# Performance work log

Measured on AMD Instinct MI355X. Metric: run time of the kernel, lower is better.

The kernel has to match this reference:

```python
import jax, jax.numpy as jnp
import numpy as np

B, Q, C, N, H, W = 2, 4096, 256, 6, 64, 96
HEADS, POINTS = 8, 4


def _grid_sample(img, grid):
    # img: [G, C, H, W]; grid: [G, P, 2] in [-1,1]
    # bilinear, align_corners=False, padding_mode='zeros' (matches F.grid_sample)
    G, Cc, Hh, Ww = img.shape
    gx = (grid[..., 0] + 1.0) * (Ww / 2.0) - 0.5
    gy = (grid[..., 1] + 1.0) * (Hh / 2.0) - 0.5
    x0f = jnp.floor(gx)
    y0f = jnp.floor(gy)
    wx = (gx - x0f)[:, None, :]
    wy = (gy - y0f)[:, None, :]
    x0 = x0f.astype(jnp.int32)
    y0 = y0f.astype(jnp.int32)
    flat = img.reshape(G, Cc, Hh * Ww)

    def gather(xi, yi):
        valid = ((xi >= 0) & (xi < Ww) & (yi >= 0) & (yi < Hh))
        idx = jnp.clip(yi, 0, Hh - 1) * Ww + jnp.clip(xi, 0, Ww - 1)
        v = jnp.take_along_axis(flat, idx[:, None, :], axis=2)  # [G,C,P]
        return v * valid[:, None, :].astype(img.dtype)

    v00 = gather(x0, y0)
    v01 = gather(x0 + 1, y0)
    v10 = gather(x0, y0 + 1)
    v11 = gather(x0 + 1, y0 + 1)
    return (v00 * (1 - wx) * (1 - wy) + v01 * wx * (1 - wy)
            + v10 * (1 - wx) * wy + v11 * wx * wy)


def setup_inputs() -> dict:
    key = jax.random.key(0)
    ks = jax.random.split(key, 12)
    query = jax.random.normal(ks[0], (B, Q, C), dtype=jnp.float32)
    query_coords = jax.random.uniform(ks[1], (B, Q, 3), dtype=jnp.float32)
    image_feats = jax.random.normal(ks[2], (B, N, C, H, W), dtype=jnp.float32)
    # realistic f-theta fisheye intrinsics for 1280x1080 images
    Kmat = np.array([[500.0, 0.0, 640.0], [0.0, 500.0, 540.0], [0.0, 0.0, 1.0]], dtype=np.float32)
    intrinsics = jnp.asarray(np.tile(Kmat, (B, N, 1, 1)))
    # inverse extrinsics: identity rotation, cameras 3m behind the voxel volume (cam_z > 0)
    E = np.tile(np.eye(4, dtype=np.float32), (B, N, 1, 1))
    for n in range(N):
        E[:, n, 0, 3] = 0.2 * n - 0.5
        E[:, n, 2, 3] = 3.0
    inv_extrinsics = jnp.asarray(E)
    s = 1.0 / np.sqrt(C)
    W_off = jax.random.normal(ks[3], (C, N * HEADS * POINTS * 2), dtype=jnp.float32) * 0.02
    b_off = jnp.zeros((N * HEADS * POINTS * 2,), dtype=jnp.float32)
    W_attn = jax.random.normal(ks[4], (C, N * HEADS * POINTS), dtype=jnp.float32) * s
    b_attn = jnp.zeros((N * HEADS * POINTS,), dtype=jnp.float32)
    W_val = jax.random.normal(ks[5], (C, C), dtype=jnp.float32) * s
    b_val = jax.random.normal(ks[6], (C,), dtype=jnp.float32) * 0.01
    W_out = jax.random.normal(ks[7], (C, C), dtype=jnp.float32) * s
    b_out = jax.random.normal(ks[8], (C,), dtype=jnp.float32) * 0.01
    return {"query": query, "query_coords": query_coords, "image_feats": image_feats,
            "intrinsics": intrinsics, "inv_extrinsics": inv_extrinsics,
            "W_off": W_off, "b_off": b_off, "W_attn": W_attn, "b_attn": b_attn,
            "W_val": W_val, "b_val": b_val, "W_out": W_out, "b_out": b_out}


def reference(query, query_coords, image_feats, intrinsics, inv_extrinsics,
              W_off, b_off, W_attn, b_attn, W_val, b_val, W_out, b_out):
    Bq, Qq, Cq = query.shape
    _, Nn, _, Hh, Ww = image_feats.shape
    hd = Cq // HEADS
    # ---- reference points: voxel coords -> world -> camera -> f-theta image ----
    xmin, ymin, zmin, xmax, ymax, zmax = -3.6, -3.0, -0.7, 3.6, 3.0, 2.5
    rx = query_coords[..., 0] * (xmax - xmin) + xmin
    ry = query_coords[..., 1] * (ymax - ymin) + ymin
    rz = query_coords[..., 2] * (zmax - zmin) + zmin
    world = jnp.stack([rx, ry, rz, jnp.ones_like(rx)], axis=-1)  # [B,Q,4]
    cam = jnp.einsum('bnij,bqj->bnqi', inv_extrinsics, world)    # [B,N,Q,4]
    cxp, cyp, czp = cam[..., 0], cam[..., 1], cam[..., 2]
    r3d = jnp.sqrt(cxp * cxp + cyp * cyp + 1e-8)
    theta = jnp.arctan2(r3d, czp)
    phi = jnp.arctan2(cyp, cxp)
    fx = intrinsics[:, :, 0, 0][..., None]
    cx0 = intrinsics[:, :, 0, 2][..., None]
    cy0 = intrinsics[:, :, 1, 2][..., None]
    r_img = fx * theta
    u = r_img * jnp.cos(phi) + cx0
    v = r_img * jnp.sin(phi) + cy0
    origH, origW = 1080, 1280
    ref = jnp.stack([2.0 * u / (origW - 1) - 1.0, 2.0 * v / (origH - 1) - 1.0], axis=-1)  # [B,N,Q,2]
    fov = ((czp > 0) & (theta < 1.372)).astype(query.dtype)      # [B,N,Q]
    # ---- offsets + attention weights ----
    offs = jnp.tanh((query @ W_off + b_off).reshape(Bq, Qq, Nn, HEADS, POINTS, 2)) * 0.5
    aw = (query @ W_attn + b_attn).reshape(Bq, Qq, Nn, HEADS, POINTS)
    aw = aw * jnp.transpose(fov, (0, 2, 1))[..., None, None]
    aw = jax.nn.softmax(aw, axis=-1)
    # ---- value projection ----
    val = jnp.einsum('bnchw,cd->bnhwd', image_feats, W_val) + b_val  # [B,N,H,W,C]
    val = val.reshape(Bq, Nn, Hh, Ww, HEADS, hd)
    # ---- sampling locations ----
    locs = ref[:, :, :, None, None, :] + jnp.transpose(offs, (0, 2, 1, 3, 4, 5))  # [B,N,Q,h,p,2]
    v_all = jnp.transpose(val, (0, 1, 4, 5, 2, 3)).reshape(Bq * Nn * HEADS, hd, Hh, Ww)
    locs_all = jnp.transpose(locs, (0, 1, 3, 2, 4, 5)).reshape(Bq * Nn * HEADS, Qq * POINTS, 2)
    sampled = _grid_sample(v_all, locs_all).reshape(Bq, Nn, HEADS, hd, Qq, POINTS)
    sampled = jnp.transpose(sampled, (0, 4, 1, 2, 5, 3))  # [B,Q,N,heads,points,hd]
    weighted = jnp.sum(sampled * aw[..., None], axis=4)   # [B,Q,N,heads,hd]
    out = weighted.sum(axis=2).reshape(Bq, Qq, Cq)
    return out @ W_out + b_out
```

## Files before the change

### kernel.cpp

```cpp
#include <hip/hip_runtime.h>
#include <math.h>

#define Bb 2
#define Qq 4096
#define Cc 256
#define Nn 6
#define Hh 64
#define Ww 96
#define HEADS 8
#define POINTS 4
#define HW (Hh*Ww)
#define BQ (Bb*Qq)

#define WS_VAL   0
#define WS_WTF   9437184
#define WS_WCHF  9469952
#define WS_WCLF  9543680
#define WS_WOTF  9617408
#define WS_LOCS  18874368
#define WS_AW    22020096
#define WS_REFF  23592960
#define WS_WSUM  23740416

typedef __attribute__((ext_vector_type(8))) short short8;
typedef __attribute__((ext_vector_type(4))) float f32x4;

__device__ __forceinline__ unsigned short f2bf(float f) {
    union { float f; unsigned u; } v; v.f = f;
    unsigned r = (v.u + 0x7fffu + ((v.u >> 16) & 1u)) >> 16;
    return (unsigned short)r;
}
__device__ __forceinline__ float bf2f(unsigned short h) { return __uint_as_float((unsigned)h << 16); }
__device__ __forceinline__ float bflo(unsigned u) { return __uint_as_float(u << 16); }
__device__ __forceinline__ float bfhi(unsigned u) { return __uint_as_float(u & 0xffff0000u); }
__device__ __forceinline__ unsigned packbf(float a, float b) {
    return (unsigned)f2bf(a) | ((unsigned)f2bf(b) << 16);
}

__global__ void prep_kernel(const float* __restrict__ qc,
                            const float* __restrict__ intr,
                            const float* __restrict__ invE,
                            float* __restrict__ reff,
                            const float* __restrict__ Wv,
                            const float* __restrict__ Wo,
                            const float* __restrict__ Wa,
                            const float* __restrict__ Wu,
                            unsigned short* __restrict__ Wtf,
                            unsigned short* __restrict__ Wchf,
                            unsigned short* __restrict__ Wclf,
                            unsigned short* __restrict__ Wotf) {
    int blk = blockIdx.x;
    int tid = threadIdx.x;
    if (blk < 32) {
        int idx = blk * 256 + tid;
        int b = idx >> 12;
        int q = idx & (Qq - 1);
        float rx = qc[idx*3+0] * 7.2f - 3.6f;
        float ry = qc[idx*3+1] * 6.0f - 3.0f;
        float rz = qc[idx*3+2] * 3.2f - 0.7f;
        for (int n = 0; n < Nn; ++n) {
            const float* E = invE + (b*Nn+n)*16;
            float camx = E[0]*rx + E[1]*ry + E[2]*rz  + E[3];
            float camy = E[4]*rx + E[5]*ry + E[6]*rz  + E[7];
            float camz = E[8]*rx + E[9]*ry + E[10]*rz + E[11];
            const float* K = intr + (b*Nn+n)*9;
            float fx = K[0], cx0 = K[2], cy0 = K[5];
            float r3d   = sqrtf(camx*camx + camy*camy + 1e-8f);
            float theta = atan2f(r3d, camz);
            float phi   = atan2f(camy, camx);
            float r_img = fx * theta;
            float u = r_img * cosf(phi) + cx0;
            float v = r_img * sinf(phi) + cy0;
            int base = ((b*Nn+n)*Qq + q)*3;
            reff[base+0] = 2.0f * u / 1279.0f - 1.0f;
            reff[base+1] = 2.0f * v / 1079.0f - 1.0f;
            reff[base+2] = (camz > 0.0f && theta < 1.372f) ? 1.0f : 0.0f;
        }
        return;
    }
    int idx = (blk - 32) * 256 + tid;
    if (idx < 65536) {
        int s = idx & 7, l = (idx >> 3) & 63, kk = (idx >> 9) & 7, t = idx >> 12;
        int n = t*16 + (l & 15);
        int k = kk*32 + (l >> 4)*8 + s;
        Wtf[idx] = f2bf(Wv[k*256 + n]);
    } else if (idx < 212992) {
        int i2 = idx - 65536;
        int s = i2 & 7, l = (i2 >> 3) & 63, kk = (i2 >> 9) & 7, t = i2 >> 12;
        int n = t*16 + (l & 15);
        int k = kk*32 + (l >> 4)*8 + s;
        float w = (n < 384) ? Wo[k*384 + n] : Wa[k*192 + (n - 384)];
        unsigned short h = f2bf(w);
        Wchf[i2] = h;
        Wclf[i2] = f2bf(w - bf2f(h));
    } else {
        int i3 = idx - 212992;
        int s = i3 & 7, l = (i3 >> 3) & 63, kk = (i3 >> 9) & 7, t = i3 >> 12;
        int n = t*16 + (l & 15);
        int k = kk*32 + (l >> 4)*8 + s;
        Wotf[i3] = f2bf(Wu[k*256 + n]);
    }
}

__global__ __launch_bounds__(512, 2) void vp_mfma_kernel(const float* __restrict__ feats,
                                                         const unsigned short* __restrict__ Wtf,
                                                         const float* __restrict__ bv,
                                                         unsigned short* __restrict__ val) {
    __shared__ __align__(16) unsigned short As[64 * 272];
    int t = threadIdx.x;
    int pix0 = blockIdx.x * 64;
    int bn = blockIdx.y;
    const float* A = feats + (size_t)bn * Cc * HW + pix0;
    int lane = t & 63, wavei = t >> 6, quad = lane >> 4, l15 = lane & 15;
    {
        int pq = t & 15;
        int oct = t >> 4;
        float va[8][4];
#pragma unroll
        for (int j = 0; j < 8; ++j)
            *(float4*)va[j] = *(const float4*)&A[(size_t)(oct*8 + j)*HW + pq*4];
#pragma unroll
        for (int e = 0; e < 4; ++e) {
            int m = pq*4 + e;
            uint4 pk;
            pk.x = packbf(va[0][e], va[1][e]);
            pk.y = packbf(va[2][e], va[3][e]);
            pk.z = packbf(va[4][e], va[5][e]);
            pk.w = packbf(va[6][e], va[7][e]);
            *(uint4*)&As[m*264 + oct*8] = pk;
        }
    }
    __syncthreads();
    int wm = wavei & 1;
    int wn = wavei >> 1;
    int r0 = wm*32 + l15, r1 = r0 + 16;
    const unsigned short* Wl = Wtf + (size_t)lane * 8;
#define VP_BOFF(nt, kk) ((size_t)(((wn*4 + (nt))*8 + (kk)) << 9))
    f32x4 acc[2][4];
#pragma unroll
    for (int i = 0; i < 2; ++i)
#pragma unroll
        for (int j = 0; j < 4; ++j) acc[i][j] = (f32x4){0.f, 0.f, 0.f, 0.f};
    short8 bA[4], bB[4];
#pragma unroll
    for (int nt = 0; nt < 4; ++nt) bA[nt] = *(const short8*)&Wl[VP_BOFF(nt, 0)];
#pragma unroll
    for (int kk = 0; kk < 8; kk += 2) {
        if (kk + 1 < 8) {
#pragma unroll
            for (int nt = 0; nt < 4; ++nt) bB[nt] = *(const short8*)&Wl[VP_BOFF(nt, kk+1)];
        }
        {
            short8 a0 = *(const short8*)&As[r0*264 + kk*32 + quad*8];
            short8 a1 = *(const short8*)&As[r1*264 + kk*32 + quad*8];
#pragma unroll
            for (int nt = 0; nt < 4; ++nt) {
                acc[0][nt] = __builtin_amdgcn_mfma_f32_16x16x32_bf16(a0, bA[nt], acc[0][nt], 0, 0, 0);
                acc[1][nt] = __builtin_amdgcn_mfma_f32_16x16x32_bf16(a1, bA[nt], acc[1][nt], 0, 0, 0);
            }
        }
        if (kk + 2 < 8) {
#pragma unroll
            for (int nt = 0; nt < 4; ++nt) bA[nt] = *(const short8*)&Wl[VP_BOFF(nt, kk+2)];
        }
        if (kk + 1 < 8) {
            int k1 = kk + 1;
            short8 a0 = *(const short8*)&As[r0*264 + k1*32 + quad*8];
            short8 a1 = *(const short8*)&As[r1*264 + k1*32 + quad*8];
#pragma unroll
            for (int nt = 0; nt < 4; ++nt) {
                acc[0][nt] = __builtin_amdgcn_mfma_f32_16x16x32_bf16(a0, bB[nt], acc[0][nt], 0, 0, 0);
                acc[1][nt] = __builtin_amdgcn_mfma_f32_16x16x32_bf16(a1, bB[nt], acc[1][nt], 0, 0, 0);
            }
        }
    }
    __syncthreads();
#pragma unroll
    for (int nt = 0; nt < 4; ++nt) {
        int n = wn*64 + nt*16 + l15;
        float bias = bv[n];
#pragma unroll
        for (int mt = 0; mt < 2; ++mt) {
#pragma unroll
            for (int r = 0; r < 4; ++r) {
                int mm = wm*32 + mt*16 + quad*4 + r;
                As[mm*272 + n] = f2bf(acc[mt][nt][r] + bias);
            }
        }
    }
    __syncthreads();
    unsigned short* dst = val + ((size_t)bn*HW + pix0)*256;
#pragma unroll
    for (int i = 0; i < 4; ++i) {
        int flat = wavei*2048 + i*512 + lane*8;
        int pix = flat >> 8, ch = flat & 255;
        *(uint4*)&dst[flat] = *(const uint4*)&As[pix*272 + ch];
    }
}

__global__ __launch_bounds__(512, 2) void qp_kernel(const float* __restrict__ query,
                                                    const unsigned short* __restrict__ Wchf,
                                                    const unsigned short* __restrict__ Wclf,
                                                    const float* __restrict__ b_off,
                                                    const float* __restrict__ b_attn,
                                                    const float* __restrict__ reff,
                                                    float* __restrict__ locs,
                                                    float* __restrict__ aw) {
    __shared__ __align__(16) unsigned short Ah[32 * 256];
    __shared__ __align__(16) unsigned short Al[32 * 256];
    int t = threadIdx.x;
    int row0 = blockIdx.x * 32;
    {
        int row = t & 31;
        int c2 = t >> 5;
        const float* src = query + (size_t)(row0 + row) * 256;
#pragma unroll
        for (int cc = 0; cc < 2; ++cc) {
            int c = c2 * 2 + cc;
            float4 v0 = *(const float4*)&src[c*8 + 0];
            float4 v1 = *(const float4*)&src[c*8 + 4];
            float f[8] = {v0.x, v0.y, v0.z, v0.w, v1.x, v1.y, v1.z, v1.w};
            unsigned short h[8], l[8];
#pragma unroll
            for (int j = 0; j < 8; ++j) {
                h[j] = f2bf(f[j]);
                l[j] = f2bf(f[j] - bf2f(h[j]));
            }
            uint4 ph, pl;
            ph.x = h[0] | ((unsigned)h[1] << 16); ph.y = h[2] | ((unsigned)h[3] << 16);
            ph.z = h[4] | ((unsigned)h[5] << 16); ph.w = h[6] | ((unsigned)h[7] << 16);
            pl.x = l[0] | ((unsigned)l[1] << 16); pl.y = l[2] | ((unsigned)l[3] << 16);
            pl.z = l[4] | ((unsigned)l[5] << 16); pl.w = l[6] | ((unsigned)l[7] << 16);
            int pos = row * 256 + ((c ^ row) << 3);
            *(uint4*)&Ah[pos] = ph;
            *(uint4*)&Al[pos] = pl;
        }
    }
    __syncthreads();
    int wave = t >> 6, lane = t & 63, quad = lane >> 4, l15 = lane & 15;
    int ms = wave & 1;
    int ng = wave >> 1;
    int arow = ms*16 + l15;
    int bq = row0 >> 12;
#pragma unroll
    for (int ib = 0; ib < 3; ++ib) {
        f32x4 acc[3];
#pragma unroll
        for (int i = 0; i < 3; ++i) acc[i] = (f32x4){0.f, 0.f, 0.f, 0.f};
        int col0 = ng*144 + ib*48;
        int tile0 = ng*9 + ib*3;
#pragma unroll
        for (int kk = 0; kk < 8; ++kk) {
            int apos = arow*256 + (((kk*4+quad) ^ arow) << 3);
            short8 a_h = *(const short8*)&Ah[apos];
            short8 a_l = *(const short8*)&Al[apos];
#pragma unroll
            for (int i = 0; i < 3; ++i) {
                bool prec = (col0 + i*16) < 384;
                size_t fb = ((size_t)((tile0 + i)*8 + kk) << 9) + lane*8;
                short8 b_h = *(const short8*)&Wchf[fb];
                acc[i] = __builtin_amdgcn_mfma_f32_16x16x32_bf16(a_h, b_h, acc[i], 0, 0, 0);
                if (prec) {
                    short8 b_l = *(const short8*)&Wclf[fb];
                    acc[i] = __builtin_amdgcn_mfma_f32_16x16x32_bf16(a_l, b_h, acc[i], 0, 0, 0);
                    acc[i] = __builtin_amdgcn_mfma_f32_16x16x32_bf16(a_h, b_l, acc[i], 0, 0, 0);
                }
            }
        }
#pragma unroll
        for (int i = 0; i < 3; ++i) {
            int tcol = col0 + i*16;
            int j = tcol + l15;
            if (tcol < 384) {
                int n_cam = j >> 6;
                int xy = j & 1;
                float bias = b_off[j];
#pragma unroll
                for (int r = 0; r < 4; ++r) {
                    int q = row0 + ms*16 + quad*4 + r;
                    int qq = q & (Qq-1);
                    float refv = reff[((bq*Nn + n_cam)*Qq + qq)*3 + xy];
                    locs[(size_t)q*384 + j] = refv + tanhf(acc[i][r] + bias) * 0.5f;
                }
            } else {
                int j2 = j - 384;
                int n_cam = j2 >> 5;
                float bias = b_attn[j2];
#pragma unroll
                for (int r = 0; r < 4; ++r) {
                    int q = row0 + ms*16 + quad*4 + r;
                    int qq = q & (Qq-1);
                    float fov = reff[((bq*Nn + n_cam)*Qq + qq)*3 + 2];
                    float lg = (acc[i][r] + bias) * fov;
                    float mx = fmaxf(lg, __shfl_xor(lg, 1));
                    mx = fmaxf(mx, __shfl_xor(mx, 2));
                    float e = expf(lg - mx);
                    float s = e + __shfl_xor(e, 1);
                    s = s + __shfl_xor(s, 2);
                    aw[(size_t)q*192 + j2] = e / s;
                }
            }
        }
    }
}

__global__ __launch_bounds__(256, 4) void samp_kernel(const unsigned short* __restrict__ val,
                                                      const float* __restrict__ locs,
                                                      const float* __restrict__ aw,
                                                      unsigned short* __restrict__ wsum) {
    __shared__ __align__(16) float swgt[4][192][4];
    __shared__ __align__(16) int   soff[4][192][4];
    int t = threadIdx.x, wv = t >> 6, lane = t & 63;
    int q = blockIdx.x * 4 + wv;
    int b = q >> 12;
#pragma unroll
    for (int j = 0; j < 3; ++j) {
        int s = lane + 64*j;
        float2 xy = *(const float2*)&locs[(size_t)q*384 + 2*s];
        float w = aw[(size_t)q*192 + s];
        float gx = (xy.x + 1.0f)*48.0f - 0.5f;
        float gy = (xy.y + 1.0f)*32.0f - 0.5f;
        float x0f = floorf(gx), y0f = floorf(gy);
        float wx = gx - x0f, wy = gy - y0f;
        int ix = (int)x0f, iy = (int)y0f;
        bool vx0 = (unsigned)ix       < (unsigned)Ww;
        bool vx1 = (unsigned)(ix + 1) < (unsigned)Ww;
        bool vy0 = (unsigned)iy       < (unsigned)Hh;
        bool vy1 = (unsigned)(iy + 1) < (unsigned)Hh;
        int ix0 = min(max(ix, 0), Ww-1), ix1 = min(max(ix+1, 0), Ww-1);
        int iy0 = min(max(iy, 0), Hh-1), iy1 = min(max(iy+1, 0), Hh-1);
        swgt[wv][s][0] = (vx0 && vy0) ? w*(1.0f-wx)*(1.0f-wy) : 0.0f;
        swgt[wv][s][1] = (vx1 && vy0) ? w*wx*(1.0f-wy)        : 0.0f;
        swgt[wv][s][2] = (vx0 && vy1) ? w*(1.0f-wx)*wy        : 0.0f;
        swgt[wv][s][3] = (vx1 && vy1) ? w*wx*wy               : 0.0f;
        soff[wv][s][0] = (iy0*Ww + ix0) * 512;
        soff[wv][s][1] = (iy0*Ww + ix1) * 512;
        soff[wv][s][2] = (iy1*Ww + ix0) * 512;
        soff[wv][s][3] = (iy1*Ww + ix1) * 512;
    }
    __syncthreads();
    int cg   = lane >> 5;
    int head = (lane >> 2) & 7;
    int oc   = lane & 3;
    int c = head*32 + oc*8;
    const char* vbase = (const char*)val + (size_t)b*Nn*HW*512 + c*2;
    float a[8] = {0.f,0.f,0.f,0.f,0.f,0.f,0.f,0.f};
#pragma unroll
    for (int n = 0; n < Nn; ++n) {
        const char* vb = vbase + (size_t)n*HW*512;
#pragma unroll
        for (int p = 0; p < POINTS; ++p) {
            int s = (n*HEADS + head)*POINTS + p;
            float2 w2 = *(const float2*)&swgt[wv][s][cg*2];
            int2   o2 = *(const int2*)&soff[wv][s][cg*2];
            uint4 u0 = *(const uint4*)(vb + o2.x);
            uint4 u1 = *(const uint4*)(vb + o2.y);
            a[0] += w2.x*bflo(u0.x); a[1] += w2.x*bfhi(u0.x);
            a[2] += w2.x*bflo(u0.y); a[3] += w2.x*bfhi(u0.y);
            a[4] += w2.x*bflo(u0.z); a[5] += w2.x*bfhi(u0.z);
            a[6] += w2.x*bflo(u0.w); a[7] += w2.x*bfhi(u0.w);
            a[0] += w2.y*bflo(u1.x); a[1] += w2.y*bfhi(u1.x);
            a[2] += w2.y*bflo(u1.y); a[3] += w2.y*bfhi(u1.y);
            a[4] += w2.y*bflo(u1.z); a[5] += w2.y*bfhi(u1.z);
            a[6] += w2.y*bflo(u1.w); a[7] += w2.y*bfhi(u1.w);
        }
    }
#pragma unroll
    for (int j = 0; j < 8; ++j) a[j] += __shfl_xor(a[j], 32);
    if (cg == 0) {
        uint4 o;
        o.x = packbf(a[0], a[1]);
        o.y = packbf(a[2], a[3]);
        o.z = packbf(a[4], a[5]);
        o.w = packbf(a[6], a[7]);
        *(uint4*)&wsum[(size_t)q*256 + c] = o;
    }
}

__global__ __launch_bounds__(256) void out_mfma_kernel(const unsigned short* __restrict__ wsum,
                                                       const unsigned short* __restrict__ Wotf,
                                                       const float* __restrict__ b_out,
                                                       float* __restrict__ out) {
    int t = threadIdx.x;
    int row0 = blockIdx.x * 64;
    int col0 = blockIdx.y * 128;
    int wave = t >> 6, lane = t & 63, quad = lane >> 4, l15 = lane & 15;
    int wm = wave & 1;
    int wn = wave >> 1;
    f32x4 acc[2][4];
#pragma unroll
    for (int i = 0; i < 2; ++i)
#pragma unroll
        for (int j = 0; j < 4; ++j) acc[i][j] = (f32x4){0.f, 0.f, 0.f, 0.f};
#pragma unroll
    for (int kk = 0; kk < 8; ++kk) {
        short8 a[2];
#pragma unroll
        for (int mt = 0; mt < 2; ++mt)
            a[mt] = *(const short8*)&wsum[(size_t)(row0 + wm*32 + mt*16 + l15)*256 + kk*32 + quad*8];
#pragma unroll
        for (int nt = 0; nt < 4; ++nt) {
            size_t fb = ((size_t)((blockIdx.y*8 + wn*4 + nt)*8 + kk) << 9) + lane*8;
            short8 bfr = *(const short8*)&Wotf[fb];
            acc[0][nt] = __builtin_amdgcn_mfma_f32_16x16x32_bf16(a[0], bfr, acc[0][nt], 0, 0, 0);
            acc[1][nt] = __builtin_amdgcn_mfma_f32_16x16x32_bf16(a[1], bfr, acc[1][nt], 0, 0, 0);
        }
    }
#pragma unroll
    for (int nt = 0; nt < 4; ++nt) {
        int col = col0 + wn*64 + nt*16 + l15;
        float bias = b_out[col];
#pragma unroll
        for (int mt = 0; mt < 2; ++mt) {
#pragma unroll
            for (int r = 0; r < 4; ++r) {
                int q = row0 + wm*32 + mt*16 + quad*4 + r;
                out[(size_t)q*256 + col] = acc[mt][nt][r] + bias;
            }
        }
    }
}

extern "C" void kernel_launch(void* const* d_in, const int* in_sizes, int n_in,
                              void* d_out, int out_size, void* d_ws, size_t ws_size,
                              hipStream_t stream) {
    const float* query  = (const float*)d_in[0];
    const float* qc     = (const float*)d_in[1];
    const float* feats  = (const float*)d_in[2];
    const float* intr   = (const float*)d_in[3];
    const float* invE   = (const float*)d_in[4];
    const float* W_off  = (const float*)d_in[5];
    const float* b_off  = (const float*)d_in[6];
    const float* W_attn = (const float*)d_in[7];
    const float* b_attn = (const float*)d_in[8];
    const float* W_val  = (const float*)d_in[9];
    const float* b_val  = (const float*)d_in[10];
    const float* W_out  = (const float*)d_in[11];
    const float* b_out  = (const float*)d_in[12];
    float* out = (float*)d_out;
    float* ws  = (float*)d_ws;
    unsigned short* val  = (unsigned short*)(ws + WS_VAL);
    unsigned short* Wtf  = (unsigned short*)(ws + WS_WTF);
    unsigned short* Wchf = (unsigned short*)(ws + WS_WCHF);
    unsigned short* Wclf = (unsigned short*)(ws + WS_WCLF);
    unsigned short* Wotf = (unsigned short*)(ws + WS_WOTF);
    float* locs = ws + WS_LOCS;
    float* aw   = ws + WS_AW;
    float* reff = ws + WS_REFF;
    unsigned short* wsum = (unsigned short*)(ws + WS_WSUM);

    hipLaunchKernelGGL(prep_kernel, dim3(1120), dim3(256), 0, stream,
                       qc, intr, invE, reff, W_val, W_off, W_attn, W_out,
                       Wtf, Wchf, Wclf, Wotf);
    hipLaunchKernelGGL(vp_mfma_kernel, dim3(HW/64, Bb*Nn), dim3(512), 0, stream,
                       feats, Wtf, b_val, val);
    hipLaunchKernelGGL(qp_kernel, dim3(BQ/32), dim3(512), 0, stream,
                       query, Wchf, Wclf, b_off, b_attn, reff, locs, aw);
    hipLaunchKernelGGL(samp_kernel, dim3(BQ/4), dim3(256), 0, stream,
                       val, locs, aw, wsum);
    hipLaunchKernelGGL(out_mfma_kernel, dim3(BQ/64, 2), dim3(256), 0, stream,
                       wsum, Wotf, b_out, out);
}
```

Before: 278.0 us.

## Store value features head-major per pixel and transpose sampling tables in LDS

The value projection now writes its output in a [B,N,HEADS,HW,32] layout rather than [B,N,HW,256], so each head's 32 channels for neighbouring pixels sit in one contiguous 64-byte row. The bilinear sampling gather indexes that per-head plane, and its shared-memory weight/offset tables change from [s][corner] to padded [corner][s]. The aim is better cache locality for the gathered corners within a head and fewer LDS bank conflicts. The catch is that the projection kernel's writes become strided 16-byte stores across heads rather than contiguous rows.

```diff
diff --git a/kernel.cpp b/kernel.cpp
--- a/kernel.cpp
+++ b/kernel.cpp
@@ -189,12 +189,13 @@
         }
     }
     __syncthreads();
-    unsigned short* dst = val + ((size_t)bn*HW + pix0)*256;
 #pragma unroll
     for (int i = 0; i < 4; ++i) {
         int flat = wavei*2048 + i*512 + lane*8;
         int pix = flat >> 8, ch = flat & 255;
-        *(uint4*)&dst[flat] = *(const uint4*)&As[pix*272 + ch];
+        int head = ch >> 5, c32 = ch & 31;
+        *(uint4*)&val[(((size_t)bn*HEADS + head)*HW + pix0 + pix)*32 + c32] =
+            *(const uint4*)&As[pix*272 + ch];
     }
 }
 
@@ -308,8 +309,8 @@
                                                       const float* __restrict__ locs,
                                                       const float* __restrict__ aw,
                                                       unsigned short* __restrict__ wsum) {
-    __shared__ __align__(16) float swgt[4][192][4];
-    __shared__ __align__(16) int   soff[4][192][4];
+    __shared__ float swgt[4][4][200];
+    __shared__ int   soff[4][4][200];
     int t = threadIdx.x, wv = t >> 6, lane = t & 63;
     int q = blockIdx.x * 4 + wv;
     int b = q >> 12;
@@ -329,45 +330,47 @@
         bool vy1 = (unsigned)(iy + 1) < (unsigned)Hh;
         int ix0 = min(max(ix, 0), Ww-1), ix1 = min(max(ix+1, 0), Ww-1);
         int iy0 = min(max(iy, 0), Hh-1), iy1 = min(max(iy+1, 0), Hh-1);
-        swgt[wv][s][0] = (vx0 && vy0) ? w*(1.0f-wx)*(1.0f-wy) : 0.0f;
-        swgt[wv][s][1] = (vx1 && vy0) ? w*wx*(1.0f-wy)        : 0.0f;
-        swgt[wv][s][2] = (vx0 && vy1) ? w*(1.0f-wx)*wy        : 0.0f;
-        swgt[wv][s][3] = (vx1 && vy1) ? w*wx*wy               : 0.0f;
-        soff[wv][s][0] = (iy0*Ww + ix0) * 512;
-        soff[wv][s][1] = (iy0*Ww + ix1) * 512;
-        soff[wv][s][2] = (iy1*Ww + ix0) * 512;
-        soff[wv][s][3] = (iy1*Ww + ix1) * 512;
+        swgt[wv][0][s] = (vx0 && vy0) ? w*(1.0f-wx)*(1.0f-wy) : 0.0f;
+        swgt[wv][1][s] = (vx1 && vy0) ? w*wx*(1.0f-wy)        : 0.0f;
+        swgt[wv][2][s] = (vx0 && vy1) ? w*(1.0f-wx)*wy        : 0.0f;
+        swgt[wv][3][s] = (vx1 && vy1) ? w*wx*wy               : 0.0f;
+        soff[wv][0][s] = (iy0*Ww + ix0) * 64;
+        soff[wv][1][s] = (iy0*Ww + ix1) * 64;
+        soff[wv][2][s] = (iy1*Ww + ix0) * 64;
+        soff[wv][3][s] = (iy1*Ww + ix1) * 64;
     }
     __syncthreads();
     int cg   = lane >> 5;
     int head = (lane >> 2) & 7;
     int oc   = lane & 3;
-    int c = head*32 + oc*8;
-    const char* vbase = (const char*)val + (size_t)b*Nn*HW*512 + c*2;
+    const char* vbase = (const char*)val + (size_t)(b*Nn*HEADS + head)*HW*64 + oc*16;
     float a[8] = {0.f,0.f,0.f,0.f,0.f,0.f,0.f,0.f};
 #pragma unroll
     for (int n = 0; n < Nn; ++n) {
-        const char* vb = vbase + (size_t)n*HW*512;
+        const char* vb = vbase + (size_t)n*HEADS*HW*64;
 #pragma unroll
         for (int p = 0; p < POINTS; ++p) {
             int s = (n*HEADS + head)*POINTS + p;
-            float2 w2 = *(const float2*)&swgt[wv][s][cg*2];
-            int2   o2 = *(const int2*)&soff[wv][s][cg*2];
-            uint4 u0 = *(const uint4*)(vb + o2.x);
-            uint4 u1 = *(const uint4*)(vb + o2.y);
-            a[0] += w2.x*bflo(u0.x); a[1] += w2.x*bfhi(u0.x);
-            a[2] += w2.x*bflo(u0.y); a[3] += w2.x*bfhi(u0.y);
-            a[4] += w2.x*bflo(u0.z); a[5] += w2.x*bfhi(u0.z);
-            a[6] += w2.x*bflo(u0.w); a[7] += w2.x*bfhi(u0.w);
-            a[0] += w2.y*bflo(u1.x); a[1] += w2.y*bfhi(u1.x);
-            a[2] += w2.y*bflo(u1.y); a[3] += w2.y*bfhi(u1.y);
-            a[4] += w2.y*bflo(u1.z); a[5] += w2.y*bfhi(u1.z);
-            a[6] += w2.y*bflo(u1.w); a[7] += w2.y*bfhi(u1.w);
+            float w0 = swgt[wv][cg*2+0][s];
+            float w1 = swgt[wv][cg*2+1][s];
+            int   o0 = soff[wv][cg*2+0][s];
+            int   o1 = soff[wv][cg*2+1][s];
+            uint4 u0 = *(const uint4*)(vb + o0);
+            uint4 u1 = *(const uint4*)(vb + o1);
+            a[0] += w0*bflo(u0.x); a[1] += w0*bfhi(u0.x);
+            a[2] += w0*bflo(u0.y); a[3] += w0*bfhi(u0.y);
+            a[4] += w0*bflo(u0.z); a[5] += w0*bfhi(u0.z);
+            a[6] += w0*bflo(u0.w); a[7] += w0*bfhi(u0.w);
+            a[0] += w1*bflo(u1.x); a[1] += w1*bfhi(u1.x);
+            a[2] += w1*bflo(u1.y); a[3] += w1*bfhi(u1.y);
+            a[4] += w1*bflo(u1.z); a[5] += w1*bfhi(u1.z);
+            a[6] += w1*bflo(u1.w); a[7] += w1*bfhi(u1.w);
         }
     }
 #pragma unroll
     for (int j = 0; j < 8; ++j) a[j] += __shfl_xor(a[j], 32);
     if (cg == 0) {
+        int c = head*32 + oc*8;
         uint4 o;
         o.x = packbf(a[0], a[1]);
         o.y = packbf(a[2], a[3]);
```

After: 265.0 us. -4.7%, faster.
